# Kernel optimization log

Hardware: AMD Instinct MI355X
Metric: run time of the kernel (lower is better)

## Reference

```python
import jax, jax.numpy as jnp
import numpy as np

CORE_DIM = 128
MEMORY_SLOTS = 64
B, S = 4, 4096


def setup_inputs() -> dict:
    key = jax.random.key(0)
    k1, k2, k3, k4, k5 = jax.random.split(key, 5)
    x = jax.random.normal(k1, (B, S, CORE_DIM), dtype=jnp.float32)
    memory_keys = jax.random.normal(k2, (MEMORY_SLOTS, CORE_DIM), dtype=jnp.float32)
    memory_ops = jax.random.normal(k3, (MEMORY_SLOTS, CORE_DIM, CORE_DIM), dtype=jnp.float32)
    # nn.Linear(core_dim, core_dim): weight [out, in], bias [out]
    bound = 1.0 / np.sqrt(CORE_DIM)
    Wq = jax.random.uniform(k4, (CORE_DIM, CORE_DIM), minval=-bound, maxval=bound, dtype=jnp.float32)
    bq = jax.random.uniform(k5, (CORE_DIM,), minval=-bound, maxval=bound, dtype=jnp.float32)
    return {"input_tensor": x, "memory_keys": memory_keys, "memory_ops": memory_ops, "Wq": Wq, "bq": bq}


def reference(input_tensor, memory_keys, memory_ops, Wq, bq):
    dim = input_tensor.shape[-1]
    # query projection: x @ Wq^T + bq
    queries = jnp.einsum('bsd,ed->bse', input_tensor, Wq) + bq
    # soft attention over memory slots
    attn_logits = jnp.einsum('bsd,md->bsm', queries, memory_keys)
    attn_weights = jax.nn.softmax(attn_logits / jnp.sqrt(jnp.float32(dim)), axis=-1)
    # fused: (sum_m attn[bsm] * ops[m]) @ x[bs]  == sum_m attn[bsm] * (ops[m] @ x[bs])
    processed = jnp.einsum('bsm,mde,bse->bsd', attn_weights, memory_ops, input_tensor)
    return processed
```

## Files before the change

### kernel.cpp

```cpp
#include <hip/hip_runtime.h>

typedef __bf16 bf16x8 __attribute__((ext_vector_type(8)));
typedef float f32x4 __attribute__((ext_vector_type(4)));
typedef unsigned int uint4v __attribute__((ext_vector_type(4)));
typedef unsigned short ushort_t;
typedef unsigned int uint_t;

#define RS 0.08838834764831845f

__device__ __forceinline__ ushort_t f2bf(float f) {
    uint_t u = __float_as_uint(f);
    u += 0x7FFFu + ((u >> 16) & 1u);
    return (ushort_t)(u >> 16);
}
__device__ __forceinline__ uint_t pack2(float a, float b) {
    return (uint_t)f2bf(a) | ((uint_t)f2bf(b) << 16);
}
union U4B8 { uint4v u; bf16x8 b; };
__device__ __forceinline__ bf16x8 as_bf(uint4v u) { U4B8 x; x.u = u; return x.b; }

__device__ __forceinline__ int xfrag(int f, int lane) {
    return f * 1072 + ((lane >> 4) * 272) + ((lane & 15) * 16);
}

__global__ __launch_bounds__(256) void prep_kernel(
    const float* __restrict__ ops, const float* __restrict__ keys,
    const float* __restrict__ Wq, const float* __restrict__ bq,
    uint4v* __restrict__ ops_sw, ushort_t* __restrict__ kp_sw,
    float* __restrict__ cb)
{
    const int tid = threadIdx.x;
    const int b = blockIdx.x;
    if (b >= 64) {
        int g = (b - 64) * 256 + tid;
        int L = g & 63, dt = (g >> 6) & 7, ks = (g >> 9) & 3, m = g >> 11;
        int d = dt * 16 + (L & 15);
        int e0 = ks * 32 + ((L >> 4) << 3);
        const float4* s = (const float4*)(ops + (((size_t)(m * 128 + d)) << 7) + e0);
        float4 v0 = s[0], v1 = s[1];
        uint4v o = { pack2(v0.x, v0.y), pack2(v0.z, v0.w),
                     pack2(v1.x, v1.y), pack2(v1.z, v1.w) };
        ops_sw[g] = o;
    } else {
        __shared__ float red[256];
        const int m = b;
        const int d = tid & 127, eh = tid >> 7;
        const float* kr = keys + m * 128 + eh * 64;
        const float* wc = Wq + (size_t)(eh * 64) * 128 + d;
        float acc = 0.f;
        #pragma unroll 8
        for (int e = 0; e < 64; ++e)
            acc = fmaf(kr[e], wc[(size_t)e * 128], acc);
        red[tid] = acc;
        __syncthreads();
        if (tid < 128) {
            float v = red[tid] + red[tid + 128];
            int ki = d >> 5, qq = (d >> 3) & 3, j = d & 7;
            kp_sw[((((ki * 4 + (m >> 4)) * 64) + (qq * 16 + (m & 15))) << 3) | j] = f2bf(v);
        } else if (tid >= 192) {
            int lane = tid - 192;
            float p = keys[m * 128 + lane] * bq[lane]
                    + keys[m * 128 + 64 + lane] * bq[64 + lane];
            #pragma unroll
            for (int off = 1; off < 64; off <<= 1) p += __shfl_xor(p, off);
            if (lane == 0) cb[m] = p;
        }
    }
}

__global__ __launch_bounds__(256, 2) void main_kernel(
    const float* __restrict__ x, const float* __restrict__ cb,
    const ushort_t* __restrict__ kp_sw, const uint4v* __restrict__ ops_sw,
    float* __restrict__ out)
{
    __shared__ __align__(16) unsigned char xs[17152];
    __shared__ float attn_f[64 * 68];

    const int tid = threadIdx.x;
    const int lane = tid & 63;
    const int w = tid >> 6;
    const int q = lane >> 4;
    const int l15 = lane & 15;
    const int tb = blockIdx.x >> 1;
    const int dh = blockIdx.x & 1;
    const int t0 = tb * 64;
    const int dtw = dh * 4 + w;

    {
        const float4* x4 = (const float4*)(x + (size_t)t0 * 128);
        #pragma unroll
        for (int it = 0; it < 4; ++it) {
            int i = it * 256 + tid;
            int t = i >> 4, kc = i & 15;
            float4 a = x4[t * 32 + kc * 2];
            float4 b2 = x4[t * 32 + kc * 2 + 1];
            uint4v o = { pack2(a.x, a.y), pack2(a.z, a.w),
                         pack2(b2.x, b2.y), pack2(b2.z, b2.w) };
            *(uint4v*)(xs + ((t >> 4) * 4 + (kc >> 2)) * 1072
                          + (kc & 3) * 272 + (t & 15) * 16) = o;
        }
    }
    __syncthreads();

    {
        f32x4 L0 = {0,0,0,0}, L1 = {0,0,0,0}, L2 = {0,0,0,0}, L3 = {0,0,0,0};
        const uint4v* kpf = (const uint4v*)kp_sw;
        #pragma unroll
        for (int ki = 0; ki < 4; ++ki) {
            bf16x8 a = *(const bf16x8*)(xs + xfrag(w * 4 + ki, lane));
            L0 = __builtin_amdgcn_mfma_f32_16x16x32_bf16(a, as_bf(kpf[(ki*4+0)*64 + lane]), L0, 0,0,0);
            L1 = __builtin_amdgcn_mfma_f32_16x16x32_bf16(a, as_bf(kpf[(ki*4+1)*64 + lane]), L1, 0,0,0);
            L2 = __builtin_amdgcn_mfma_f32_16x16x32_bf16(a, as_bf(kpf[(ki*4+2)*64 + lane]), L2, 0,0,0);
            L3 = __builtin_amdgcn_mfma_f32_16x16x32_bf16(a, as_bf(kpf[(ki*4+3)*64 + lane]), L3, 0,0,0);
        }
        float c0 = cb[l15], c1 = cb[16 + l15], c2 = cb[32 + l15], c3 = cb[48 + l15];
        #pragma unroll
        for (int r = 0; r < 4; ++r) {
            float v0 = (L0[r] + c0) * RS;
            float v1 = (L1[r] + c1) * RS;
            float v2 = (L2[r] + c2) * RS;
            float v3 = (L3[r] + c3) * RS;
            float mx = fmaxf(fmaxf(v0, v1), fmaxf(v2, v3));
            #pragma unroll
            for (int off = 1; off < 16; off <<= 1) mx = fmaxf(mx, __shfl_xor(mx, off));
            float e0 = __expf(v0 - mx), e1 = __expf(v1 - mx),
                  e2 = __expf(v2 - mx), e3 = __expf(v3 - mx);
            float sm = e0 + e1 + e2 + e3;
            #pragma unroll
            for (int off = 1; off < 16; off <<= 1) sm += __shfl_xor(sm, off);
            float inv = 1.0f / sm;
            int t = w * 16 + q * 4 + r;
            attn_f[(     l15) * 68 + t] = e0 * inv;
            attn_f[(16 + l15) * 68 + t] = e1 * inv;
            attn_f[(32 + l15) * 68 + t] = e2 * inv;
            attn_f[(48 + l15) * 68 + t] = e3 * inv;
        }
    }

    bf16x8 A[4][4];
    #pragma unroll
    for (int tf = 0; tf < 4; ++tf)
        #pragma unroll
        for (int ki = 0; ki < 4; ++ki)
            A[tf][ki] = *(const bf16x8*)(xs + xfrag(tf * 4 + ki, lane));

    __syncthreads();

    const uint4v* ob = ops_sw + (size_t)dtw * 64 + lane;
    f32x4 C[4] = {};
    uint4v B[4][4];
    #pragma unroll
    for (int ki = 0; ki < 4; ++ki) {
        B[0][ki] = ob[ki * 512];
        B[1][ki] = ob[2048 + ki * 512];
    }

    #pragma unroll 4
    for (int ml = 0; ml < 64; ++ml) {
        const int cur = ml & 3, nxt = (ml + 2) & 3;
        if (ml < 62) {
            const uint4v* pn = ob + (size_t)(ml + 2) * 2048;
            #pragma unroll
            for (int ki = 0; ki < 4; ++ki) B[nxt][ki] = pn[ki * 512];
        }
        f32x4 S[4] = {};
        #pragma unroll
        for (int ki = 0; ki < 4; ++ki) {
            bf16x8 bfrag = as_bf(B[cur][ki]);
            #pragma unroll
            for (int tf = 0; tf < 4; ++tf)
                S[tf] = __builtin_amdgcn_mfma_f32_16x16x32_bf16(A[tf][ki], bfrag, S[tf], 0,0,0);
        }
        #pragma unroll
        for (int tf = 0; tf < 4; ++tf) {
            f32x4 af = *(const f32x4*)&attn_f[ml * 68 + tf * 16 + q * 4];
            #pragma unroll
            for (int r = 0; r < 4; ++r)
                C[tf][r] = fmaf(af[r], S[tf][r], C[tf][r]);
        }
    }

    float* op = out + (size_t)t0 * 128 + dh * 64 + w * 16 + l15;
    #pragma unroll
    for (int tf = 0; tf < 4; ++tf)
        #pragma unroll
        for (int r = 0; r < 4; ++r)
            op[(size_t)(tf * 16 + q * 4 + r) * 128] = C[tf][r];
}

extern "C" void kernel_launch(void* const* d_in, const int* in_sizes, int n_in,
                              void* d_out, int out_size, void* d_ws, size_t ws_size,
                              hipStream_t stream)
{
    const float* x    = (const float*)d_in[0];
    const float* keys = (const float*)d_in[1];
    const float* ops  = (const float*)d_in[2];
    const float* Wq   = (const float*)d_in[3];
    const float* bq   = (const float*)d_in[4];
    float* out = (float*)d_out;

    char* ws = (char*)d_ws;
    uint4v*   ops_sw = (uint4v*)ws;
    ushort_t* kp_sw  = (ushort_t*)(ws + 2097152);
    float*    cb     = (float*)(ws + 2097152 + 16384);

    prep_kernel<<<576, 256, 0, stream>>>(ops, keys, Wq, bq, ops_sw, kp_sw, cb);
    main_kernel<<<512, 256, 0, stream>>>(x, cb, kp_sw, ops_sw, out);
}
```

Before: 108.3 us.

## Double block tile to 128 tokens and stage ops slices through LDS via async loads

Each block now processes 128 tokens with 512 threads, so each ops slice loaded from global memory is shared by two token groups of waves. Ops fragments are staged into a double-buffered LDS buffer using global_load_lds instead of register prefetch, and the prep kernel writes them in a new order to match. The goal is to halve global ops traffic per token and overlap loads with MFMA work. In exchange it adds a block-wide barrier per slot pair, uses more LDS (which may limit occupancy), and launches half as many blocks.

```diff
diff --git a/kernel.cpp b/kernel.cpp
--- a/kernel.cpp
+++ b/kernel.cpp
@@ -21,6 +21,12 @@
 
 __device__ __forceinline__ int xfrag(int f, int lane) {
     return f * 1072 + ((lane >> 4) * 272) + ((lane & 15) * 16);
+}
+
+__device__ __forceinline__ void gload16(const void* g, void* l) {
+    __builtin_amdgcn_global_load_lds(
+        (const __attribute__((address_space(1))) void*)g,
+        (__attribute__((address_space(3))) void*)l, 16, 0, 0);
 }
 
 __global__ __launch_bounds__(256) void prep_kernel(
@@ -40,7 +46,8 @@
         float4 v0 = s[0], v1 = s[1];
         uint4v o = { pack2(v0.x, v0.y), pack2(v0.z, v0.w),
                      pack2(v1.x, v1.y), pack2(v1.z, v1.w) };
-        ops_sw[g] = o;
+        int h = m * 2048 + (dt >> 2) * 1024 + ks * 256 + (dt & 3) * 64 + L;
+        ops_sw[h] = o;
     } else {
         __shared__ float red[256];
         const int m = b;
@@ -68,13 +75,14 @@
     }
 }
 
-__global__ __launch_bounds__(256, 2) void main_kernel(
+__global__ __launch_bounds__(512, 2) void main_kernel(
     const float* __restrict__ x, const float* __restrict__ cb,
     const ushort_t* __restrict__ kp_sw, const uint4v* __restrict__ ops_sw,
     float* __restrict__ out)
 {
-    __shared__ __align__(16) unsigned char xs[17152];
-    __shared__ float attn_f[64 * 68];
+    __shared__ __align__(16) unsigned char xs[34304];
+    __shared__ float attn_f[64 * 132];
+    __shared__ __align__(16) uint4v bb[2][2048];
 
     const int tid = threadIdx.x;
     const int lane = tid & 63;
@@ -83,14 +91,15 @@
     const int l15 = lane & 15;
     const int tb = blockIdx.x >> 1;
     const int dh = blockIdx.x & 1;
-    const int t0 = tb * 64;
-    const int dtw = dh * 4 + w;
+    const int t0 = tb * 128;
+    const int dtp = w & 3;
+    const int tg = w >> 2;
 
     {
         const float4* x4 = (const float4*)(x + (size_t)t0 * 128);
         #pragma unroll
         for (int it = 0; it < 4; ++it) {
-            int i = it * 256 + tid;
+            int i = it * 512 + tid;
             int t = i >> 4, kc = i & 15;
             float4 a = x4[t * 32 + kc * 2];
             float4 b2 = x4[t * 32 + kc * 2 + 1];
@@ -130,10 +139,10 @@
             for (int off = 1; off < 16; off <<= 1) sm += __shfl_xor(sm, off);
             float inv = 1.0f / sm;
             int t = w * 16 + q * 4 + r;
-            attn_f[(     l15) * 68 + t] = e0 * inv;
-            attn_f[(16 + l15) * 68 + t] = e1 * inv;
-            attn_f[(32 + l15) * 68 + t] = e2 * inv;
-            attn_f[(48 + l15) * 68 + t] = e3 * inv;
+            attn_f[(     l15) * 132 + t] = e0 * inv;
+            attn_f[(16 + l15) * 132 + t] = e1 * inv;
+            attn_f[(32 + l15) * 132 + t] = e2 * inv;
+            attn_f[(48 + l15) * 132 + t] = e3 * inv;
         }
     }
 
@@ -142,50 +151,55 @@
     for (int tf = 0; tf < 4; ++tf)
         #pragma unroll
         for (int ki = 0; ki < 4; ++ki)
-            A[tf][ki] = *(const bf16x8*)(xs + xfrag(tf * 4 + ki, lane));
-
+            A[tf][ki] = *(const bf16x8*)(xs + xfrag(tg * 16 + tf * 4 + ki, lane));
+
+    const int sb = w * 64 + lane;
+    auto stage = [&](int pair, int buf) {
+        #pragma unroll
+        for (int j = 0; j < 4; ++j) {
+            int slot = pair * 2 + (j >> 1);
+            const uint4v* g = ops_sw + ((size_t)(slot * 2 + dh) << 10)
+                            + (j & 1) * 512 + sb;
+            gload16((const void*)g, (void*)&bb[buf][j * 512 + (w << 6)]);
+        }
+    };
+
+    stage(0, 0);
     __syncthreads();
 
-    const uint4v* ob = ops_sw + (size_t)dtw * 64 + lane;
     f32x4 C[4] = {};
-    uint4v B[4][4];
-    #pragma unroll
-    for (int ki = 0; ki < 4; ++ki) {
-        B[0][ki] = ob[ki * 512];
-        B[1][ki] = ob[2048 + ki * 512];
-    }
-
-    #pragma unroll 4
-    for (int ml = 0; ml < 64; ++ml) {
-        const int cur = ml & 3, nxt = (ml + 2) & 3;
-        if (ml < 62) {
-            const uint4v* pn = ob + (size_t)(ml + 2) * 2048;
-            #pragma unroll
-            for (int ki = 0; ki < 4; ++ki) B[nxt][ki] = pn[ki * 512];
-        }
-        f32x4 S[4] = {};
-        #pragma unroll
-        for (int ki = 0; ki < 4; ++ki) {
-            bf16x8 bfrag = as_bf(B[cur][ki]);
-            #pragma unroll
-            for (int tf = 0; tf < 4; ++tf)
-                S[tf] = __builtin_amdgcn_mfma_f32_16x16x32_bf16(A[tf][ki], bfrag, S[tf], 0,0,0);
-        }
-        #pragma unroll
-        for (int tf = 0; tf < 4; ++tf) {
-            f32x4 af = *(const f32x4*)&attn_f[ml * 68 + tf * 16 + q * 4];
-            #pragma unroll
-            for (int r = 0; r < 4; ++r)
-                C[tf][r] = fmaf(af[r], S[tf][r], C[tf][r]);
-        }
-    }
-
-    float* op = out + (size_t)t0 * 128 + dh * 64 + w * 16 + l15;
+    #pragma unroll 2
+    for (int p = 0; p < 32; ++p) {
+        if (p < 31) stage(p + 1, (p + 1) & 1);
+        const uint4v* bbuf = &bb[p & 1][0];
+        #pragma unroll
+        for (int sl = 0; sl < 2; ++sl) {
+            const int m = p * 2 + sl;
+            f32x4 S[4] = {};
+            #pragma unroll
+            for (int ki = 0; ki < 4; ++ki) {
+                bf16x8 bfrag = as_bf(bbuf[sl * 1024 + ki * 256 + dtp * 64 + lane]);
+                #pragma unroll
+                for (int tf = 0; tf < 4; ++tf)
+                    S[tf] = __builtin_amdgcn_mfma_f32_16x16x32_bf16(A[tf][ki], bfrag, S[tf], 0,0,0);
+            }
+            #pragma unroll
+            for (int tf = 0; tf < 4; ++tf) {
+                f32x4 af = *(const f32x4*)&attn_f[m * 132 + tg * 64 + tf * 16 + q * 4];
+                #pragma unroll
+                for (int r = 0; r < 4; ++r)
+                    C[tf][r] = fmaf(af[r], S[tf][r], C[tf][r]);
+            }
+        }
+        __syncthreads();
+    }
+
+    float* op = out + (size_t)t0 * 128 + dh * 64 + dtp * 16 + l15;
     #pragma unroll
     for (int tf = 0; tf < 4; ++tf)
         #pragma unroll
         for (int r = 0; r < 4; ++r)
-            op[(size_t)(tf * 16 + q * 4 + r) * 128] = C[tf][r];
+            op[(size_t)(tg * 64 + tf * 16 + q * 4 + r) * 128] = C[tf][r];
 }
 
 extern "C" void kernel_launch(void* const* d_in, const int* in_sizes, int n_in,
@@ -205,5 +219,5 @@
     float*    cb     = (float*)(ws + 2097152 + 16384);
 
     prep_kernel<<<576, 256, 0, stream>>>(ops, keys, Wq, bq, ops_sw, kp_sw, cb);
-    main_kernel<<<512, 256, 0, stream>>>(x, cb, kp_sw, ops_sw, out);
-}
+    main_kernel<<<256, 512, 0, stream>>>(x, cb, kp_sw, ops_sw, out);
+}
```

After: 115.7 us. +6.9%, slower.
